# Optimization experiments

Hardware: AMD Instinct MI355X
Metric: run time of the kernel (lower is better)

## Reference

```python
import jax, jax.numpy as jnp
import numpy as np
from jax import lax

B, DIM, H, W = 2, 96, 256, 256
HEADS, WIN = 4, 8
HID = int(DIM * 2.66)  # ffn hidden_features = 255


def setup_inputs() -> dict:
    key = jax.random.key(0)
    ks = jax.random.split(key, 8)
    s = 0.02
    return {
        "x": jax.random.normal(ks[0], (B, DIM, H, W), jnp.float32),
        "to_hidden_w": jax.random.normal(ks[1], (6 * DIM, DIM), jnp.float32) * s,
        "to_hidden_dw_w": jax.random.normal(ks[2], (6 * DIM, 1, 3, 3), jnp.float32) * s,
        "project_out_w": jax.random.normal(ks[3], (DIM, 2 * DIM), jnp.float32) * s,
        "temperature": jnp.ones((HEADS, 1, 1, 1), jnp.float32),
        "norm1_w": jnp.ones((DIM,), jnp.float32),
        "norm2_w": jnp.ones((DIM,), jnp.float32),
        "ffn_in_w": jax.random.normal(ks[4], (2 * HID, DIM), jnp.float32) * s,
        "ffn_dw_w": jax.random.normal(ks[5], (2 * HID, 1, 3, 3), jnp.float32) * s,
        "ffn_out_w": jax.random.normal(ks[6], (DIM, HID), jnp.float32) * s,
    }


def _ln_biasfree(x, w):
    # BiasFree_LayerNorm over channel dim (torch var over last dim of b,(hw),c)
    v = jnp.var(x, axis=1, keepdims=True)
    return x / jnp.sqrt(v + 1e-5) * w[None, :, None, None]


def _conv1x1(x, w):
    return jnp.einsum('bchw,oc->bohw', x, w)


def _dwconv3(x, w):
    return lax.conv_general_dilated(x, w, (1, 1), [(1, 1), (1, 1)],
                                    feature_group_count=x.shape[1],
                                    dimension_numbers=('NCHW', 'OIHW', 'NCHW'))


def _to_patch(t):
    # b (head c) (h p1) (w p2) -> b head (h w) c (p1 p2)
    b, hc, hh, ww = t.shape
    c, h, w = hc // HEADS, hh // WIN, ww // WIN
    t = t.reshape(b, HEADS, c, h, WIN, w, WIN)
    t = t.transpose(0, 1, 3, 5, 2, 4, 6)
    return t.reshape(b, HEADS, h * w, c, WIN * WIN)


def _from_patch(t, hh, ww):
    # b head (h w) c (p1 p2) -> b (head c) (h p1) (w p2)
    b, hd, hw, c, pp = t.shape
    h, w = hh // WIN, ww // WIN
    t = t.reshape(b, hd, h, w, c, WIN, WIN)
    t = t.transpose(0, 1, 4, 2, 5, 3, 6)
    return t.reshape(b, hd * c, hh, ww)


def _attn(x, to_hidden_w, to_hidden_dw_w, project_out_w, temperature):
    hh, ww = x.shape[-2:]
    hidden = _dwconv3(_conv1x1(x, to_hidden_w), to_hidden_dw_w)
    q, k, v = jnp.split(hidden, 3, axis=1)
    qf = jnp.fft.rfft(_to_patch(q), axis=-1)
    kf = jnp.fft.rfft(_to_patch(k), axis=-1)
    vf = jnp.fft.rfft(_to_patch(v), axis=-1)
    attn = jnp.einsum('bhpcf,bhpcg->bhpfg', qf, kf) * temperature[None]
    nrm = jnp.sqrt(jnp.sum(jnp.abs(attn) ** 2, axis=-1, keepdims=True))  # complex last-dim vector norm
    attn = attn / nrm
    out = jnp.einsum('bhpfg,bhpcg->bhpcf', attn, vf)  # (attn @ vf^T)^T -> b head p c f
    out = jnp.fft.irfft(out, n=WIN * WIN, axis=-1)
    return _conv1x1(_from_patch(out, hh, ww), project_out_w)


def _ffn(x, w_in, w_dw, w_out):
    t = _dwconv3(_conv1x1(x, w_in), w_dw)
    x1, x2 = jnp.split(t, 2, axis=1)
    return _conv1x1(jax.nn.gelu(x1, approximate=False) * x2, w_out)


def reference(x, to_hidden_w, to_hidden_dw_w, project_out_w, temperature,
              norm1_w, norm2_w, ffn_in_w, ffn_dw_w, ffn_out_w):
    x = x + _attn(_ln_biasfree(x, norm1_w), to_hidden_w, to_hidden_dw_w,
                  project_out_w, temperature)
    x = x + _ffn(_ln_biasfree(x, norm2_w), ffn_in_w, ffn_dw_w, ffn_out_w)
    return x
```

## Files before the change

kernel.cpp:

```cpp
#include <hip/hip_runtime.h>
#include <hip/hip_bf16.h>
#include <math.h>

#define HW 65536
typedef __hip_bfloat16 bf16;
typedef __attribute__((ext_vector_type(8))) short short8;
typedef __attribute__((ext_vector_type(4))) float float4v;

__device__ __forceinline__ float bf2f(bf16 h) { return __bfloat162float(h); }
__device__ __forceinline__ bf16  f2bf(float f) { return __float2bfloat16(f); }
__device__ __forceinline__ float bflo(unsigned u){ return __uint_as_float(u << 16); }
__device__ __forceinline__ float bfhi(unsigned u){ return __uint_as_float(u & 0xffff0000u); }
__device__ __forceinline__ float bits2f(unsigned short u){ return __uint_as_float(((unsigned)u) << 16); }
__device__ __forceinline__ unsigned short f2bfbits(float f){
  bf16 h = __float2bfloat16(f);
  unsigned short u; __builtin_memcpy(&u, &h, 2); return u;
}
__device__ __forceinline__ bool io_is_f32(const unsigned short* tflag) {
  return tflag[0] == 0;
}
#define C64 0.09817477042468103f

__global__ __launch_bounds__(256) void convert_params(
    const void* p1, const void* p2, const void* p3, const void* p4,
    const void* p5, const void* p6, const void* p7, const void* p8,
    const void* p9, bf16* dst) {
  int i = blockIdx.x * 256 + threadIdx.x;
  if (i >= 157042) return;
  bool f32 = io_is_f32((const unsigned short*)p4);
  #define RD(src, j) (f32 ? ((const float*)(src))[j] : bits2f(((const unsigned short*)(src))[j]))
  float v;
  if      (i < 55296)  { v = RD(p1, i) * RD(p5, i % 96); }
  else if (i < 60480)  { v = RD(p2, i - 55296); }
  else if (i < 78912)  { v = RD(p3, i - 60480); }
  else if (i < 78916)  { v = RD(p4, i - 78912); }
  else if (i < 127876) { int j = i - 78916;  v = RD(p7, j) * RD(p6, j % 96); }
  else if (i < 132466) { v = RD(p8, i - 127876); }
  else {
    int j = i - 132466;
    int o = j >> 8, c = j & 255;
    v = (c < 255) ? RD(p9, o*255 + c) : 0.f;
  }
  #undef RD
  dst[i] = f2bf(v);
}

template<bool EXT>
__global__ __launch_bounds__(256) void ln_pre(const void* __restrict__ in,
                                              bf16* __restrict__ out, size_t eoff,
                                              const unsigned short* __restrict__ tflag) {
  int t = blockIdx.x * 256 + threadIdx.x;
  int p = t >> 1;
  int half = t & 1;
  const bool f32 = EXT && io_is_f32(tflag);
  float v[48];
  float s = 0.f, s2 = 0.f;
  #pragma unroll
  for (int j = 0; j < 48; ++j) {
    size_t off = (size_t)(half*48 + j) * HW + p;
    float xv = EXT ? (f32 ? ((const float*)in)[eoff + off]
                          : bits2f(((const unsigned short*)in)[eoff + off]))
                   : bits2f(((const unsigned short*)in)[off]);
    v[j] = xv; s += xv; s2 += xv*xv;
  }
  s  += __shfl_xor(s, 1);
  s2 += __shfl_xor(s2, 1);
  float mean = s * (1.f/96.f);
  float var  = s2 * (1.f/96.f) - mean*mean;
  float inv  = rsqrtf(fmaxf(var, 0.f) + 1e-5f);
  #pragma unroll
  for (int j = 0; j < 48; ++j)
    out[(size_t)(half*48 + j) * HW + p] = f2bf(v[j] * inv);
}

template<int CIN, int K32, int KP, int PT, int OT, int WAVES, bool RES,
         bool RESEXT, bool OUTEXT, bool PERM>
__global__ __launch_bounds__(WAVES*64) void conv_mfma(
    const bf16* __restrict__ in, const bf16* __restrict__ w,
    const void* __restrict__ res,
    void* __restrict__ out, size_t eoff,
    const unsigned short* __restrict__ tflag, int cout) {
  constexpr int BT = WAVES * 64;
  constexpr int NT = PT / 16;
  constexpr int MT = OT / (16 * WAVES);
  constexpr int SOS = PT + 8;
  __shared__ __align__(16) unsigned short SH[PT*KP + OT*KP];
  unsigned short (*in_lds)[KP] = (unsigned short(*)[KP])SH;
  unsigned short (*w_lds)[KP]  = (unsigned short(*)[KP])(SH + PT*KP);
  const int tid = threadIdx.x;
  const int p0 = blockIdx.x * PT;
  const int ob = blockIdx.y * OT;
  const bool iof32 = (RESEXT || OUTEXT) ? io_is_f32(tflag) : false;
  const unsigned short* inu = (const unsigned short*)in;
  const unsigned short* wu  = (const unsigned short*)w;

  for (int i = tid; i < CIN*(PT/8); i += BT) {
    int c = i / (PT/8), p8 = (i % (PT/8)) * 8;
    uint4 v = *(const uint4*)&inu[(size_t)c*HW + p0 + p8];
    unsigned short* b = &in_lds[p8][c];
    b[0]    = (unsigned short)(v.x);
    b[KP]   = (unsigned short)(v.x >> 16);
    b[2*KP] = (unsigned short)(v.y);
    b[3*KP] = (unsigned short)(v.y >> 16);
    b[4*KP] = (unsigned short)(v.z);
    b[5*KP] = (unsigned short)(v.z >> 16);
    b[6*KP] = (unsigned short)(v.w);
    b[7*KP] = (unsigned short)(v.w >> 16);
  }
  for (int i = tid; i < OT*(K32/8); i += BT) {
    int ol = i / (K32/8), cb = (i % (K32/8)) * 8;
    int o = ob + ol;
    uint4 v = make_uint4(0u, 0u, 0u, 0u);
    if (o < cout) v = *(const uint4*)&wu[(size_t)o*K32 + cb];
    *(uint4*)&w_lds[ol][cb] = v;
  }
  if (K32 > CIN) {
    for (int i = tid; i < (K32 - CIN) * PT; i += BT)
      in_lds[i % PT][CIN + i / PT] = 0;
  }
  __syncthreads();

  const int lane = tid & 63, wave = tid >> 6;
  const int col = lane & 15, quad = lane >> 4;
  float4v acc[MT][NT];
  #pragma unroll
  for (int mt = 0; mt < MT; ++mt)
    #pragma unroll
    for (int nt = 0; nt < NT; ++nt)
      acc[mt][nt] = (float4v){0.f, 0.f, 0.f, 0.f};

  #pragma unroll
  for (int ks = 0; ks < K32/32; ++ks) {
    const int kb = ks*32 + quad*8;
    short8 a[MT];
    #pragma unroll
    for (int mt = 0; mt < MT; ++mt)
      a[mt] = *(const short8*)&w_lds[(wave + WAVES*mt)*16 + col][kb];
    #pragma unroll
    for (int nt = 0; nt < NT; ++nt) {
      short8 bfr = *(const short8*)&in_lds[nt*16 + col][kb];
      #pragma unroll
      for (int mt = 0; mt < MT; ++mt)
        acc[mt][nt] = __builtin_amdgcn_mfma_f32_16x16x32_bf16(a[mt], bfr, acc[mt][nt], 0, 0, 0);
    }
  }

  __syncthreads();
  unsigned short* Sout = SH;
  #pragma unroll
  for (int mt = 0; mt < MT; ++mt) {
    #pragma unroll
    for (int nt = 0; nt < NT; ++nt) {
      const int p = nt*16 + col;
      #pragma unroll
      for (int r = 0; r < 4; ++r) {
        int ol = (wave + WAVES*mt)*16 + quad*4 + r;
        Sout[ol*SOS + p] = f2bfbits(acc[mt][nt][r]);
      }
    }
  }
  __syncthreads();

  for (int j = tid; j < OT*(PT/8); j += BT) {
    int ol = j / (PT/8), seg = j % (PT/8);
    int o = ob + ol;
    if (o >= cout) continue;
    int p = seg*8;
    int nat;
    if (PERM) {
      int pg = p0 + p;
      int window = pg >> 6, e = pg & 63;
      nat = (((window >> 5)*8 + (e >> 3)) << 8) + ((window & 31) << 3);
    } else {
      nat = p0 + p;
    }
    size_t oi = (size_t)o * HW + nat;
    uint4 hv = *(const uint4*)&Sout[ol*SOS + p];
    if (!RES && !(OUTEXT)) {
      *(uint4*)((unsigned short*)out + oi) = hv;
      continue;
    }
    float f0=bflo(hv.x), f1=bfhi(hv.x), f2=bflo(hv.y), f3=bfhi(hv.y);
    float f4=bflo(hv.z), f5=bfhi(hv.z), f6=bflo(hv.w), f7=bfhi(hv.w);
    if (RES) {
      if (RESEXT && iof32) {
        const float* rp = (const float*)res + eoff + oi;
        float4 r0 = *(const float4*)rp;
        float4 r1 = *(const float4*)(rp + 4);
        f0+=r0.x; f1+=r0.y; f2+=r0.z; f3+=r0.w;
        f4+=r1.x; f5+=r1.y; f6+=r1.z; f7+=r1.w;
      } else {
        const unsigned short* rp = (const unsigned short*)res + (RESEXT ? eoff + oi : oi);
        uint4 rv = *(const uint4*)rp;
        f0+=bflo(rv.x); f1+=bfhi(rv.x); f2+=bflo(rv.y); f3+=bfhi(rv.y);
        f4+=bflo(rv.z); f5+=bfhi(rv.z); f6+=bflo(rv.w); f7+=bfhi(rv.w);
      }
    }
    if (OUTEXT && iof32) {
      float* op = (float*)out + eoff + oi;
      *(float4*)op       = make_float4(f0, f1, f2, f3);
      *(float4*)(op + 4) = make_float4(f4, f5, f6, f7);
    } else {
      uint4 ov;
      ov.x = f2bfbits(f0) | ((unsigned)f2bfbits(f1) << 16);
      ov.y = f2bfbits(f2) | ((unsigned)f2bfbits(f3) << 16);
      ov.z = f2bfbits(f4) | ((unsigned)f2bfbits(f5) << 16);
      ov.w = f2bfbits(f6) | ((unsigned)f2bfbits(f7) << 16);
      *(uint4*)((unsigned short*)out + (OUTEXT ? eoff + oi : oi)) = ov;
    }
  }
}

__device__ __forceinline__ void dw9x8(const unsigned short* __restrict__ pin,
                                      const bf16* __restrict__ w,
                                      int y, int x0, float* __restrict__ o) {
  float wv[9];
  #pragma unroll
  for (int i = 0; i < 9; ++i) wv[i] = bf2f(w[i]);
  float r[3][10];
  #pragma unroll
  for (int dy = 0; dy < 3; ++dy) {
    int yy = y + dy - 1;
    if (yy < 0 || yy > 255) {
      #pragma unroll
      for (int j = 0; j < 10; ++j) r[dy][j] = 0.f;
    } else {
      const unsigned short* row = pin + yy*256 + x0;
      uint4 q = *(const uint4*)row;
      r[dy][1] = bflo(q.x); r[dy][2] = bfhi(q.x);
      r[dy][3] = bflo(q.y); r[dy][4] = bfhi(q.y);
      r[dy][5] = bflo(q.z); r[dy][6] = bfhi(q.z);
      r[dy][7] = bflo(q.w); r[dy][8] = bfhi(q.w);
      r[dy][0] = (x0 > 0)   ? bits2f(row[-1]) : 0.f;
      r[dy][9] = (x0 < 248) ? bits2f(row[8])  : 0.f;
    }
  }
  #pragma unroll
  for (int j = 0; j < 8; ++j) {
    float s = 0.f;
    #pragma unroll
    for (int dy = 0; dy < 3; ++dy)
      #pragma unroll
      for (int dx = 0; dx < 3; ++dx)
        s += r[dy][j+dx] * wv[dy*3+dx];
    o[j] = s;
  }
}

__global__ __launch_bounds__(256) void dwconv_gate_v8(const bf16* __restrict__ in,
                                                      const bf16* __restrict__ w,
                                                      bf16* __restrict__ out) {
  int t = blockIdx.x * 256 + threadIdx.x;
  int g8 = t & 8191;
  int c  = t >> 13;
  int y  = g8 >> 5;
  int x0 = (g8 & 31) << 3;
  float d1[8], d2[8];
  dw9x8((const unsigned short*)in + ((size_t)c << 16),         w + c*9,       y, x0, d1);
  dw9x8((const unsigned short*)in + ((size_t)(c+255) << 16),   w + (c+255)*9, y, x0, d2);
  unsigned short ob[8];
  #pragma unroll
  for (int j = 0; j < 8; ++j) {
    float g = 0.5f * d1[j] * (1.f + erff(d1[j] * 0.70710678118654752f)) * d2[j];
    ob[j] = f2bfbits(g);
  }
  uint4 ov;
  ov.x = ob[0] | ((unsigned)ob[1] << 16);
  ov.y = ob[2] | ((unsigned)ob[3] << 16);
  ov.z = ob[4] | ((unsigned)ob[5] << 16);
  ov.w = ob[6] | ((unsigned)ob[7] << 16);
  *(uint4*)((unsigned short*)out + ((size_t)c << 16) + y*256 + x0) = ov;
}

__global__ __launch_bounds__(512, 8) void fft_attn_mfma(const bf16* __restrict__ hid,
                                                        const bf16* __restrict__ temp,
                                                        bf16* __restrict__ outP,
                                                        const bf16* __restrict__ wdw) {
  constexpr int RS  = 68;
  constexpr int MS  = 100;
  constexpr int RAW = 0;
  constexpr int WFo = 9792;
  constexpr int QAo = 0;
  constexpr int KB1 = 4800;
  constexpr int KB2 = 9600;
  constexpr int VAo = 14400;
  constexpr int AB1 = 0;
  constexpr int AB2 = 4800;
  constexpr int OAo = 9600;
  constexpr int WIo = 0;
  constexpr int PoutO = 14400;
  __shared__ __align__(16) unsigned short S[19200];
  __shared__ float inv_s[48];
  __shared__ float2 tw2f[64];

  const int tid = threadIdx.x;
  const int lane = tid & 63, wave = tid >> 6;
  const int col = lane & 15, quad = lane >> 4;

  const int bid = blockIdx.x;
  const int sw  = ((bid & 7) << 9) | (bid >> 3);
  const int head = sw >> 10;
  const int patch = sw & 1023;
  const int y0 = (patch >> 5) * 8, x0 = (patch & 31) * 8;
  const float tscale = bf2f(temp[head]);
  const unsigned short* hidu = (const unsigned short*)hid;

  if (tid < 64) {
    float rev = (float)tid * 0.015625f;
    tw2f[tid] = make_float2(__builtin_amdgcn_cosf(rev), __builtin_amdgcn_sinf(rev));
  }
  for (int i = tid; i < 1152; i += 512) {
    int tc = i >> 3, wr = i & 7;
    int chan = (tc/48)*192 + head*48 + (tc%48);
    float o[8];
    dw9x8(hidu + ((size_t)chan << 16), wdw + chan*9, y0 + wr, x0, o);
    unsigned short* d = &S[RAW + tc*RS + wr*8];
    uint2 lo = make_uint2(f2bfbits(o[0]) | ((unsigned)f2bfbits(o[1]) << 16),
                          f2bfbits(o[2]) | ((unsigned)f2bfbits(o[3]) << 16));
    uint2 hi = make_uint2(f2bfbits(o[4]) | ((unsigned)f2bfbits(o[5]) << 16),
                          f2bfbits(o[6]) | ((unsigned)f2bfbits(o[7]) << 16));
    *(uint2*)d       = lo;
    *(uint2*)(d + 4) = hi;
  }
  for (int i = tid; i < 80*64; i += 512) {
    int n = i >> 6, e = i & 63;
    float v = 0.f;
    if (n < 33)      v =  __builtin_amdgcn_cosf((float)((n*e) & 63) * 0.015625f);
    else if (n < 66) v = -__builtin_amdgcn_sinf((float)(((n-33)*e) & 63) * 0.015625f);
    S[WFo + n*RS + e] = f2bfbits(v);
  }
  __syncthreads();

  float4v dacc[6];
  #pragma unroll
  for (int k = 0; k < 6; ++k) {
    int ti = wave + 8*k;
    if (ti < 45) {
      int mt = ti/5, nt = ti%5;
      const unsigned short* arow = &S[RAW + (mt*16+col)*RS];
      const unsigned short* brow = &S[WFo + (nt*16+col)*RS];
      float4v acc = (float4v){0.f,0.f,0.f,0.f};
      #pragma unroll
      for (int ks = 0; ks < 2; ++ks)
        acc = __builtin_amdgcn_mfma_f32_16x16x32_bf16(
            *(const short8*)(arow + ks*32 + quad*8),
            *(const short8*)(brow + ks*32 + quad*8), acc, 0,0,0);
      dacc[k] = acc;
    }
  }
  __syncthreads();

  #pragma unroll
  for (int k = 0; k < 6; ++k) {
    int ti = wave + 8*k;
    if (ti < 45) {
      int mt = ti/5, nt = ti%5;
      int n = nt*16 + col;
      if (n < 66) {
        bool isre = n < 33;
        int f = isre ? n : n - 33;
        float4v acc = dacc[k];
        #pragma unroll
        for (int r = 0; r < 4; ++r) {
          int m = mt*16 + quad*4 + r;
          int t = m/48, c = m - t*48;
          unsigned short vb = f2bfbits(acc[r]);
          if (t == 0) {
            S[QAo + f*MS + (isre ? c : 48 + c)] = vb;
          } else if (t == 1) {
            if (isre) { S[KB1 + f*MS + c] = vb;  S[KB2 + f*MS + 48 + c] = vb; }
            else      { S[KB2 + f*MS + c] = vb;  S[KB1 + f*MS + 48 + c] = f2bfbits(-acc[r]); }
          } else {
            S[VAo + c*MS + (isre ? f : 48 + f)] = vb;
          }
        }
      }
    }
  }
  for (int i = tid; i < 1500; i += 512) {
    S[QAo + 3300 + i] = 0; S[KB1 + 3300 + i] = 0; S[KB2 + 3300 + i] = 0;
  }
  for (int i = tid; i < 48*30; i += 512) {
    int r = i/30, cc = i - r*30;
    S[VAo + r*MS + (cc < 15 ? 33 + cc : 66 + cc)] = 0;
  }
  __syncthreads();

  float4v qacc[3];
  #pragma unroll
  for (int k = 0; k < 3; ++k) {
    int ti = wave + 8*k;
    if (ti < 18) {
      int mat = ti/9, rem = ti - mat*9, mt = rem/3, nt = rem%3;
      const unsigned short* arow = &S[QAo + (mt*16+col)*MS];
      const unsigned short* brow = &S[(mat ? KB2 : KB1) + (nt*16+col)*MS];
      float4v acc = (float4v){0.f,0.f,0.f,0.f};
      #pragma unroll
      for (int ks = 0; ks < 3; ++ks)
        acc = __builtin_amdgcn_mfma_f32_16x16x32_bf16(
            *(const short8*)(arow + ks*32 + quad*8),
            *(const short8*)(brow + ks*32 + quad*8), acc, 0,0,0);
      qacc[k] = acc;
    }
  }
  __syncthreads();

  #pragma unroll
  for (int k = 0; k < 3; ++k) {
    int ti = wave + 8*k;
    if (ti < 18) {
      int mat = ti/9, rem = ti - mat*9, mt = rem/3, nt = rem%3;
      int g = nt*16 + col;
      #pragma unroll
      for (int r = 0; r < 4; ++r) {
        int f = mt*16 + quad*4 + r;
        float v = qacc[k][r] * tscale;
        unsigned short vb = f2bfbits(v);
        if (mat == 0) { S[AB1 + f*MS + g] = vb;  S[AB2 + f*MS + 48 + g] = vb; }
        else          { S[AB2 + f*MS + g] = vb;  S[AB1 + f*MS + 48 + g] = f2bfbits(-v); }
      }
    }
  }
  __syncthreads();

  float4v vacc[3];
  #pragma unroll
  for (int k = 0; k < 3; ++k) {
    int ti = wave + 8*k;
    if (ti < 18) {
      int mat = ti/9, rem = ti - mat*9, mt = rem/3, nt = rem%3;
      const unsigned short* arow = &S[VAo + (mt*16+col)*MS];
      const unsigned short* brow = &S[(mat ? AB2 : AB1) + (nt*16+col)*MS];
      float4v acc = (float4v){0.f,0.f,0.f,0.f};
      #pragma unroll
      for (int ks = 0; ks < 3; ++ks)
        acc = __builtin_amdgcn_mfma_f32_16x16x32_bf16(
            *(const short8*)(arow + ks*32 + quad*8),
            *(const short8*)(brow + ks*32 + quad*8), acc, 0,0,0);
      vacc[k] = acc;
    }
  }
  if (tid < 48) {
    const unsigned short* r1 = &S[AB1 + tid*MS];
    const unsigned short* r2 = &S[AB2 + tid*MS];
    float s = 0.f;
    #pragma unroll
    for (int g8 = 0; g8 < 4; ++g8) {
      uint2 a = *(const uint2*)(r1 + g8*8);
      uint2 b = *(const uint2*)(r2 + g8*8);
      float a0=bflo(a.x),a1=bfhi(a.x),a2=bflo(a.y),a3=bfhi(a.y);
      float b0=bflo(b.x),b1=bfhi(b.x),b2=bflo(b.y),b3=bfhi(b.y);
      s += a0*a0+a1*a1+a2*a2+a3*a3 + b0*b0+b1*b1+b2*b2+b3*b3;
      uint2 c = *(const uint2*)(r1 + g8*8 + 4);
      uint2 d = *(const uint2*)(r2 + g8*8 + 4);
      float c0=bflo(c.x),c1=bfhi(c.x),c2=bflo(c.y),c3=bfhi(c.y);
      float d0=bflo(d.x),d1=bfhi(d.x),d2=bflo(d.y),d3=bfhi(d.y);
      s += c0*c0+c1*c1+c2*c2+c3*c3 + d0*d0+d1*d1+d2*d2+d3*d3;
    }
    float xr = bits2f(r1[32]);
    float xi = bits2f(r2[32]);
    s += xr*xr + xi*xi;
    inv_s[tid] = 1.f / fmaxf(sqrtf(s), 1e-30f);
  }
  __syncthreads();

  #pragma unroll
  for (int k = 0; k < 3; ++k) {
    int ti = wave + 8*k;
    if (ti < 18) {
      int mat = ti/9, rem = ti - mat*9, mt = rem/3, nt = rem%3;
      int f = nt*16 + col;
      float iv = inv_s[f];
      #pragma unroll
      for (int r = 0; r < 4; ++r) {
        int c = mt*16 + quad*4 + r;
        S[OAo + c*MS + (mat ? 48 + f : f)] = f2bfbits(vacc[k][r] * iv);
      }
    }
  }
  for (int i = tid; i < 64*96; i += 512) {
    int e = i/96, k = i - e*96;
    float v = 0.f;
    if (k < 33) {
      if (k == 0)       v = 0.015625f;
      else if (k == 32) v = (e & 1) ? -0.015625f : 0.015625f;
      else              v = 0.03125f * tw2f[(k*e) & 63].x;
    } else if (k >= 48 && k < 81) {
      int f2 = k - 48;
      if (f2 != 0 && f2 != 32) v = -0.03125f * tw2f[(f2*e) & 63].y;
    }
    S[WIo + e*MS + k] = f2bfbits(v);
  }
  __syncthreads();

  #pragma unroll
  for (int k = 0; k < 2; ++k) {
    int ti = wave + 8*k;
    if (ti < 12) {
      int mt = ti >> 2, nt = ti & 3;
      const unsigned short* arow = &S[OAo + (mt*16+col)*MS];
      const unsigned short* brow = &S[WIo + (nt*16+col)*MS];
      float4v acc = (float4v){0.f,0.f,0.f,0.f};
      #pragma unroll
      for (int ks = 0; ks < 3; ++ks)
        acc = __builtin_amdgcn_mfma_f32_16x16x32_bf16(
            *(const short8*)(arow + ks*32 + quad*8),
            *(const short8*)(brow + ks*32 + quad*8), acc, 0,0,0);
      int e = nt*16 + col;
      #pragma unroll
      for (int r = 0; r < 4; ++r) {
        int c = mt*16 + quad*4 + r;
        S[PoutO + c*72 + e] = f2bfbits(acc[r]);
      }
    }
  }
  __syncthreads();

  {
    unsigned short* outPu = (unsigned short*)outP;
    for (int j = tid; j < 384; j += 512) {
      int c = j >> 3, seg = j & 7;
      uint4 hv = *(const uint4*)&S[PoutO + c*72 + seg*8];
      *(uint4*)(outPu + (size_t)(head*48 + c)*HW + patch*64 + seg*8) = hv;
    }
  }
}

extern "C" void kernel_launch(void* const* d_in, const int* in_sizes, int n_in,
                              void* d_out, int out_size, void* d_ws, size_t ws_size,
                              hipStream_t stream) {
  const void* x   = d_in[0];
  const unsigned short* tflag = (const unsigned short*)d_in[4];

  char* ws = (char*)d_ws;
  bf16* A   = (bf16*)(ws);
  bf16* Bb  = (bf16*)(ws + 75497472);
  bf16* X1  = (bf16*)(ws + 150994944);
  bf16* prm = (bf16*)(ws + 176160768);
  bf16* Xn  = Bb;

  bf16* w_hid     = prm + 0;
  bf16* w_hid_dw  = prm + 55296;
  bf16* w_proj    = prm + 60480;
  bf16* tempc     = prm + 78912;
  bf16* w_ffn_in  = prm + 78916;
  bf16* w_ffn_dw  = prm + 127876;
  bf16* w_ffn_out = prm + 132466;

  convert_params<<<614, 256, 0, stream>>>(d_in[1], d_in[2], d_in[3], d_in[4],
                                          d_in[5], d_in[6], d_in[7], d_in[8],
                                          d_in[9], prm);

  for (int b = 0; b < 2; ++b) {
    size_t eoff = (size_t)b * 96 * HW;
    bf16* X1b = X1 + eoff;

    ln_pre<true><<<512, 256, 0, stream>>>(x, Xn, eoff, tflag);
    conv_mfma<96,96,104,128,128, 8, false,false,false,false>
        <<<dim3(512,5), 512, 0, stream>>>(Xn, w_hid, nullptr, A, 0, tflag, 576);
    fft_attn_mfma<<<4096, 512, 0, stream>>>(A, tempc, Bb , w_hid_dw);
    conv_mfma<192,192,200,128,64, 4, true,true,false,true>
        <<<dim3(512,2), 256, 0, stream>>>(Bb, w_proj, x, X1b, eoff, tflag, 96);

    ln_pre<false><<<512, 256, 0, stream>>>(X1b, Xn, 0, tflag);
    conv_mfma<96,96,104,128,128, 8, false,false,false,false>
        <<<dim3(512,4), 512, 0, stream>>>(Xn, w_ffn_in, nullptr, A, 0, tflag, 510);
    dwconv_gate_v8<<<8160, 256, 0, stream>>>(A, w_ffn_dw, Bb );
    conv_mfma<255,256,264,64,64, 4, true,false,true,false>
        <<<dim3(1024,2), 256, 0, stream>>>(Bb, w_ffn_out, X1b, d_out, eoff, tflag, 96);
  }
}
```

Measured before the change: 1.065 ms.

## Swizzle conv1x1 input LDS layout and write FFT-attn output directly to global

The conv1x1 MFMA kernel now stores the transposed input tile in LDS with a per-row rotation of the channel index, so the scattered transpose writes and the short8 fragment reads hit fewer bank conflicts. In the FFT attention kernel the final inverse-DFT MFMA result goes straight to global memory as scalar bf16 stores. This drops the LDS staging buffer, one barrier and the vectorized copy-out. The twiddle table is also removed and the cos/sin values are computed inline. The trade-offs are extra index arithmetic in the conv kernel, narrow uncoalesced 2-byte global stores, and more transcendental instructions.

After: 970.3 us (median of 2 runs). 1.1x faster.

```diff
diff --git a/kernel.cpp b/kernel.cpp
--- a/kernel.cpp
+++ b/kernel.cpp
@@ -94,18 +94,23 @@
   const unsigned short* inu = (const unsigned short*)in;
   const unsigned short* wu  = (const unsigned short*)w;
 
+  #define ROTS(r) ({ int _s = (((r) >> 3) << 3); if (_s >= K32) _s -= K32; _s; })
+
   for (int i = tid; i < CIN*(PT/8); i += BT) {
     int c = i / (PT/8), p8 = (i % (PT/8)) * 8;
     uint4 v = *(const uint4*)&inu[(size_t)c*HW + p0 + p8];
-    unsigned short* b = &in_lds[p8][c];
-    b[0]    = (unsigned short)(v.x);
-    b[KP]   = (unsigned short)(v.x >> 16);
-    b[2*KP] = (unsigned short)(v.y);
-    b[3*KP] = (unsigned short)(v.y >> 16);
-    b[4*KP] = (unsigned short)(v.z);
-    b[5*KP] = (unsigned short)(v.z >> 16);
-    b[6*KP] = (unsigned short)(v.w);
-    b[7*KP] = (unsigned short)(v.w >> 16);
+    unsigned short e[8];
+    e[0] = (unsigned short)(v.x); e[1] = (unsigned short)(v.x >> 16);
+    e[2] = (unsigned short)(v.y); e[3] = (unsigned short)(v.y >> 16);
+    e[4] = (unsigned short)(v.z); e[5] = (unsigned short)(v.z >> 16);
+    e[6] = (unsigned short)(v.w); e[7] = (unsigned short)(v.w >> 16);
+    #pragma unroll
+    for (int j = 0; j < 8; ++j) {
+      int row = p8 + j;
+      int pc = c + ROTS(row);
+      if (pc >= K32) pc -= K32;
+      in_lds[row][pc] = e[j];
+    }
   }
   for (int i = tid; i < OT*(K32/8); i += BT) {
     int ol = i / (K32/8), cb = (i % (K32/8)) * 8;
@@ -115,8 +120,12 @@
     *(uint4*)&w_lds[ol][cb] = v;
   }
   if (K32 > CIN) {
-    for (int i = tid; i < (K32 - CIN) * PT; i += BT)
-      in_lds[i % PT][CIN + i / PT] = 0;
+    for (int i = tid; i < (K32 - CIN) * PT; i += BT) {
+      int row = i % PT, lc = CIN + i / PT;
+      int pc = lc + ROTS(row);
+      if (pc >= K32) pc -= K32;
+      in_lds[row][pc] = 0;
+    }
   }
   __syncthreads();
 
@@ -138,12 +147,16 @@
       a[mt] = *(const short8*)&w_lds[(wave + WAVES*mt)*16 + col][kb];
     #pragma unroll
     for (int nt = 0; nt < NT; ++nt) {
-      short8 bfr = *(const short8*)&in_lds[nt*16 + col][kb];
+      const int row = nt*16 + col;
+      int pkb = kb + ROTS(row);
+      if (pkb >= K32) pkb -= K32;
+      short8 bfr = *(const short8*)&in_lds[row][pkb];
       #pragma unroll
       for (int mt = 0; mt < MT; ++mt)
         acc[mt][nt] = __builtin_amdgcn_mfma_f32_16x16x32_bf16(a[mt], bfr, acc[mt][nt], 0, 0, 0);
     }
   }
+  #undef ROTS
 
   __syncthreads();
   unsigned short* Sout = SH;
@@ -288,10 +301,8 @@
   constexpr int AB2 = 4800;
   constexpr int OAo = 9600;
   constexpr int WIo = 0;
-  constexpr int PoutO = 14400;
   __shared__ __align__(16) unsigned short S[19200];
   __shared__ float inv_s[48];
-  __shared__ float2 tw2f[64];
 
   const int tid = threadIdx.x;
   const int lane = tid & 63, wave = tid >> 6;
@@ -305,10 +316,6 @@
   const float tscale = bf2f(temp[head]);
   const unsigned short* hidu = (const unsigned short*)hid;
 
-  if (tid < 64) {
-    float rev = (float)tid * 0.015625f;
-    tw2f[tid] = make_float2(__builtin_amdgcn_cosf(rev), __builtin_amdgcn_sinf(rev));
-  }
   for (int i = tid; i < 1152; i += 512) {
     int tc = i >> 3, wr = i & 7;
     int chan = (tc/48)*192 + head*48 + (tc%48);
@@ -484,44 +491,37 @@
     if (k < 33) {
       if (k == 0)       v = 0.015625f;
       else if (k == 32) v = (e & 1) ? -0.015625f : 0.015625f;
-      else              v = 0.03125f * tw2f[(k*e) & 63].x;
+      else              v = 0.03125f * __builtin_amdgcn_cosf((float)((k*e) & 63) * 0.015625f);
     } else if (k >= 48 && k < 81) {
       int f2 = k - 48;
-      if (f2 != 0 && f2 != 32) v = -0.03125f * tw2f[(f2*e) & 63].y;
+      if (f2 != 0 && f2 != 32) v = -0.03125f * __builtin_amdgcn_sinf((float)((f2*e) & 63) * 0.015625f);
     }
     S[WIo + e*MS + k] = f2bfbits(v);
-  }
-  __syncthreads();
-
-  #pragma unroll
-  for (int k = 0; k < 2; ++k) {
-    int ti = wave + 8*k;
-    if (ti < 12) {
-      int mt = ti >> 2, nt = ti & 3;
-      const unsigned short* arow = &S[OAo + (mt*16+col)*MS];
-      const unsigned short* brow = &S[WIo + (nt*16+col)*MS];
-      float4v acc = (float4v){0.f,0.f,0.f,0.f};
-      #pragma unroll
-      for (int ks = 0; ks < 3; ++ks)
-        acc = __builtin_amdgcn_mfma_f32_16x16x32_bf16(
-            *(const short8*)(arow + ks*32 + quad*8),
-            *(const short8*)(brow + ks*32 + quad*8), acc, 0,0,0);
-      int e = nt*16 + col;
-      #pragma unroll
-      for (int r = 0; r < 4; ++r) {
-        int c = mt*16 + quad*4 + r;
-        S[PoutO + c*72 + e] = f2bfbits(acc[r]);
-      }
-    }
   }
   __syncthreads();
 
   {
     unsigned short* outPu = (unsigned short*)outP;
-    for (int j = tid; j < 384; j += 512) {
-      int c = j >> 3, seg = j & 7;
-      uint4 hv = *(const uint4*)&S[PoutO + c*72 + seg*8];
-      *(uint4*)(outPu + (size_t)(head*48 + c)*HW + patch*64 + seg*8) = hv;
+    #pragma unroll
+    for (int k = 0; k < 2; ++k) {
+      int ti = wave + 8*k;
+      if (ti < 12) {
+        int mt = ti >> 2, nt = ti & 3;
+        const unsigned short* arow = &S[OAo + (mt*16+col)*MS];
+        const unsigned short* brow = &S[WIo + (nt*16+col)*MS];
+        float4v acc = (float4v){0.f,0.f,0.f,0.f};
+        #pragma unroll
+        for (int ks = 0; ks < 3; ++ks)
+          acc = __builtin_amdgcn_mfma_f32_16x16x32_bf16(
+              *(const short8*)(arow + ks*32 + quad*8),
+              *(const short8*)(brow + ks*32 + quad*8), acc, 0,0,0);
+        int e = nt*16 + col;
+        #pragma unroll
+        for (int r = 0; r < 4; ++r) {
+          int c = mt*16 + quad*4 + r;
+          outPu[(size_t)(head*48 + c)*HW + patch*64 + e] = f2bfbits(acc[r]);
+        }
+      }
     }
   }
 }
```
